# Performance work log

Measured on AMD Instinct MI355X. Metric: run time of the kernel, lower is better.

## Reference

```python
import jax, jax.numpy as jnp
import numpy as np
import math

N_LEVELS = 16
F = 2
LOG2_T = 19
T = 1 << LOG2_T  # 524288 hashmap rows
BASE, FINEST = 16, 512
# b computed in float32 like torch.exp((log(512)-log(16))/15)
B_GROWTH = float(np.exp((np.log(np.float32(FINEST)) - np.log(np.float32(BASE))) / np.float32(N_LEVELS - 1)))
RES = [math.floor(BASE * B_GROWTH ** i) for i in range(N_LEVELS)]
SIZES = [(r + 1) ** 3 if r ** 3 < T else T for r in RES]
OFFS = np.concatenate([[0], np.cumsum(SIZES)]).tolist()
TOTAL_ROWS = OFFS[-1]  # 5269629
# corner order (i,j,k) for i,j,k in {0,1}, i outermost -> matches torch grid_offset
CORNER_OFF = np.array([[i, j, k] for i in (0, 1) for j in (0, 1) for k in (0, 1)], dtype=np.int32)
PRIMES = np.array([1, 2654435761, 805459861], dtype=np.uint32)
N_POINTS = 1048576


def setup_inputs() -> dict:
    key = jax.random.key(0)
    k1, k2 = jax.random.split(key)
    x = jax.random.uniform(k1, (N_POINTS, 3), dtype=jnp.float32, minval=-1.0, maxval=1.0)
    # nn.init.uniform_(-1e-4, 1e-4) on every level's embedding table
    tables = jax.random.uniform(k2, (TOTAL_ROWS, F), dtype=jnp.float32, minval=-1e-4, maxval=1e-4)
    return {"x": x, "tables": tables}


def _level_embed(x, table, res):
    # x: (B,3) in [-1,1]; table: (rows,F); res: python int (static)
    xc = jnp.clip(x, -1.0, 1.0)
    grid = jnp.float32(2.0 / res)  # (box_max-box_min)/resolution
    bl = jnp.floor((xc + 1.0) / grid).astype(jnp.int32)  # (B,3) bottom-left voxel
    vmin = bl.astype(x.dtype) * grid - 1.0               # voxel_min_vertex
    # original uses unclamped x for interpolation weights
    w = (x - vmin) / grid                                # (B,3)
    corners = bl[:, None, :] + jnp.asarray(CORNER_OFF)   # (B,8,3)
    if res ** 3 < T:
        # one-to-one hash: i*res^2 + j*res + k
        idx = corners[..., 0] * (res * res) + corners[..., 1] * res + corners[..., 2]
    else:
        # spatial hash with uint32 wraparound multiplication (matches torch int32 wrap)
        c = corners.astype(jnp.uint32)
        h = (c[..., 0] * PRIMES[0]) ^ (c[..., 1] * PRIMES[1]) ^ (c[..., 2] * PRIMES[2])
        idx = (h & jnp.uint32(T - 1)).astype(jnp.int32)
    e = table[idx]  # (B,8,F) gather
    wx, wy, wz = w[:, 0:1], w[:, 1:2], w[:, 2:3]
    c00 = e[:, 0] * (1 - wx) + e[:, 4] * wx
    c01 = e[:, 1] * (1 - wx) + e[:, 5] * wx
    c10 = e[:, 2] * (1 - wx) + e[:, 6] * wx
    c11 = e[:, 3] * (1 - wx) + e[:, 7] * wx
    c0 = c00 * (1 - wy) + c10 * wy
    c1 = c01 * (1 - wy) + c11 * wy
    return c0 * (1 - wz) + c1 * wz  # (B,F)


def reference(x, tables):
    outs = []
    for i in range(N_LEVELS):
        tab = jax.lax.slice_in_dim(tables, OFFS[i], OFFS[i + 1], axis=0)
        outs.append(_level_embed(x, tab, RES[i]))
    return jnp.concatenate(outs, axis=-1)  # (B, n_levels*F) = (B,32)
```

## Files before the change

### kernel.cpp

```cpp
#include <hip/hip_runtime.h>

#define NLVL 16
#define T_MASK ((1u << 19) - 1)
#define NBIN 32768

typedef float v2f __attribute__((ext_vector_type(2)));
typedef float v4f __attribute__((ext_vector_type(4)));

__constant__ int c_res[NLVL] = {16, 20, 25, 32, 40, 50, 64, 80,
                                101, 128, 161, 203, 256, 322, 406, 512};
__constant__ int c_off[NLVL] = {0, 4913, 14174, 31750, 67687, 136608, 269259, 543884,
                                1075325, 1599613, 2123901, 2648189, 3172477, 3696765, 4221053, 4745341};
__constant__ float c_grid[NLVL] = {
    (float)(2.0 / 16.0),  (float)(2.0 / 20.0),  (float)(2.0 / 25.0),  (float)(2.0 / 32.0),
    (float)(2.0 / 40.0),  (float)(2.0 / 50.0),  (float)(2.0 / 64.0),  (float)(2.0 / 80.0),
    (float)(2.0 / 101.0), (float)(2.0 / 128.0), (float)(2.0 / 161.0), (float)(2.0 / 203.0),
    (float)(2.0 / 256.0), (float)(2.0 / 322.0), (float)(2.0 / 406.0), (float)(2.0 / 512.0)};

constexpr int kRes[8] = {16, 20, 25, 32, 40, 50, 64, 80};
constexpr int kOff[8] = {0, 4913, 14174, 31750, 67687, 136608, 269259, 543884};
constexpr float kGrid[8] = {
    (float)(2.0 / 16.0), (float)(2.0 / 20.0), (float)(2.0 / 25.0), (float)(2.0 / 32.0),
    (float)(2.0 / 40.0), (float)(2.0 / 50.0), (float)(2.0 / 64.0), (float)(2.0 / 80.0)};

__device__ __forceinline__ void dim_setup(float xv, float grid, int& b, float& w) {
    float xc = fminf(fmaxf(xv, -1.0f), 1.0f);
    float fb = floorf((xc + 1.0f) / grid);
    b = (int)fb;
    float vmin = fb * grid - 1.0f;
    w = (xv - vmin) / grid;
}

__device__ __forceinline__ unsigned part1by2(unsigned v) {
    v &= 0x3ff;
    v = (v | (v << 16)) & 0x030000FFu;
    v = (v | (v << 8))  & 0x0300F00Fu;
    v = (v | (v << 4))  & 0x030C30C3u;
    v = (v | (v << 2))  & 0x09249249u;
    return v;
}

__device__ __forceinline__ unsigned bin3(float a, float b, float c) {
    int ba = (int)floorf((a + 1.0f) * 16.0f); ba = ba < 0 ? 0 : (ba > 31 ? 31 : ba);
    int bb = (int)floorf((b + 1.0f) * 16.0f); bb = bb < 0 ? 0 : (bb > 31 ? 31 : bb);
    int bc = (int)floorf((c + 1.0f) * 16.0f); bc = bc < 0 ? 0 : (bc > 31 ? 31 : bc);
    return part1by2((unsigned)ba) | (part1by2((unsigned)bb) << 1) | (part1by2((unsigned)bc) << 2);
}

__global__ __launch_bounds__(256) void hist_kernel(const float* __restrict__ x,
                                                   unsigned* __restrict__ hist, int n) {
    int p = (int)blockIdx.x * 256 + (int)threadIdx.x;
    if (p >= n) return;
    float a = x[3 * p], b = x[3 * p + 1], c = x[3 * p + 2];
    atomicAdd(&hist[bin3(a, b, c)], 1u);
}

__global__ __launch_bounds__(1024) void scan_kernel(const unsigned* __restrict__ hist,
                                                    unsigned* __restrict__ base) {
    __shared__ unsigned part[1024];
    const int t = (int)threadIdx.x;
    unsigned s = 0;
#pragma unroll
    for (int i = 0; i < NBIN / 1024; ++i) s += hist[t * (NBIN / 1024) + i];
    part[t] = s;
    __syncthreads();
    for (int off = 1; off < 1024; off <<= 1) {
        unsigned v = (t >= off) ? part[t - off] : 0u;
        __syncthreads();
        part[t] += v;
        __syncthreads();
    }
    unsigned run = part[t] - s;
    for (int i = 0; i < NBIN / 1024; ++i) {
        unsigned h = hist[t * (NBIN / 1024) + i];
        base[t * (NBIN / 1024) + i] = run;
        run += h;
    }
}

__global__ __launch_bounds__(256) void scatter_kernel(const float* __restrict__ x,
                                                      unsigned* __restrict__ base,
                                                      v4f* __restrict__ pts, int n) {
    int p = (int)blockIdx.x * 256 + (int)threadIdx.x;
    if (p >= n) return;
    float a = x[3 * p], b = x[3 * p + 1], c = x[3 * p + 2];
    unsigned slot = atomicAdd(&base[bin3(a, b, c)], 1u);
    v4f v; v.x = a; v.y = b; v.z = c; v.w = __int_as_float(p);
    pts[slot] = v;
}

__global__ __launch_bounds__(256) void gather_hash(const v4f* __restrict__ pts,
                                                   const float* __restrict__ tables,
                                                   v2f* __restrict__ ws2, int n) {
    const int level = (int)(blockIdx.x & 7) + 8;
    const int p = (int)(blockIdx.x >> 3) * 256 + (int)threadIdx.x;
    if (p >= n) return;

    const v4f pt = __builtin_nontemporal_load(&pts[p]);
    const float grid = c_grid[level];
    const v2f* __restrict__ tab = reinterpret_cast<const v2f*>(tables) + c_off[level];

    int bx, by, bz;
    float wx, wy, wz;
    dim_setup(pt.x, grid, bx, wx);
    dim_setup(pt.y, grid, by, wy);
    dim_setup(pt.z, grid, bz, wz);

    const unsigned hx0 = (unsigned)bx, hx1 = (unsigned)(bx + 1);
    const unsigned hy0 = (unsigned)by * 2654435761u;
    const unsigned hy1 = (unsigned)(by + 1) * 2654435761u;
    const unsigned hz0 = (unsigned)bz * 805459861u;
    const unsigned hz1 = (unsigned)(bz + 1) * 805459861u;
    v2f e0 = tab[(hx0 ^ hy0 ^ hz0) & T_MASK];
    v2f e1 = tab[(hx0 ^ hy0 ^ hz1) & T_MASK];
    v2f e2 = tab[(hx0 ^ hy1 ^ hz0) & T_MASK];
    v2f e3 = tab[(hx0 ^ hy1 ^ hz1) & T_MASK];
    v2f e4 = tab[(hx1 ^ hy0 ^ hz0) & T_MASK];
    v2f e5 = tab[(hx1 ^ hy0 ^ hz1) & T_MASK];
    v2f e6 = tab[(hx1 ^ hy1 ^ hz0) & T_MASK];
    v2f e7 = tab[(hx1 ^ hy1 ^ hz1) & T_MASK];

    const float ox = 1.0f - wx, oy = 1.0f - wy, oz = 1.0f - wz;
    v2f c00 = e0 * ox + e4 * wx;
    v2f c01 = e1 * ox + e5 * wx;
    v2f c10 = e2 * ox + e6 * wx;
    v2f c11 = e3 * ox + e7 * wx;
    v2f c0 = c00 * oy + c10 * wy;
    v2f c1 = c01 * oy + c11 * wy;
    v2f r = c0 * oz + c1 * wz;

    __builtin_nontemporal_store(r, &ws2[(size_t)(level - 8) * n + p]);
}

#define ROWSTRIDE 36
__global__ __launch_bounds__(256, 4) void dense_finish(const v4f* __restrict__ pts,
                                                       const float* __restrict__ tables,
                                                       const v2f* __restrict__ ws2,
                                                       float* __restrict__ out, int n) {
    __shared__ float lrow[256 * ROWSTRIDE];
    __shared__ int lorg[256];

    const int nb = (int)gridDim.x;
    const int bid = (int)blockIdx.x;
    const int q = nb >> 3, r = nb & 7;
    const int xcd = bid & 7, j = bid >> 3;
    const int nbid = (xcd < r) ? xcd * (q + 1) + j : r * (q + 1) + (xcd - r) * q + j;
    const int tid = (int)threadIdx.x;
    const int base_p = nbid * 256;
    const int p = base_p + tid;

    if (p < n) {
        v2f h[8];
#pragma unroll
        for (int l = 0; l < 8; ++l)
            h[l] = __builtin_nontemporal_load(&ws2[(size_t)l * n + p]);

        const v4f pt = __builtin_nontemporal_load(&pts[p]);
        lorg[tid] = __float_as_int(pt.w);

        v2f d[8];
#pragma unroll
        for (int l = 0; l < 8; ++l) {
            const int res = kRes[l];
            const float grid = kGrid[l];
            const v2f* __restrict__ tab = reinterpret_cast<const v2f*>(tables) + kOff[l];
            int bx, by, bz;
            float wx, wy, wz;
            dim_setup(pt.x, grid, bx, wx);
            dim_setup(pt.y, grid, by, wy);
            dim_setup(pt.z, grid, bz, wz);
            const int r2 = res * res;
            const int base = bx * r2 + by * res + bz;
            v2f e0 = tab[base];            v2f e1 = tab[base + 1];
            v2f e2 = tab[base + res];      v2f e3 = tab[base + res + 1];
            v2f e4 = tab[base + r2];       v2f e5 = tab[base + r2 + 1];
            v2f e6 = tab[base + r2 + res]; v2f e7 = tab[base + r2 + res + 1];
            const float ox = 1.0f - wx, oy = 1.0f - wy, oz = 1.0f - wz;
            v2f c00 = e0 * ox + e4 * wx;
            v2f c01 = e1 * ox + e5 * wx;
            v2f c10 = e2 * ox + e6 * wx;
            v2f c11 = e3 * ox + e7 * wx;
            v2f c0 = c00 * oy + c10 * wy;
            v2f c1 = c01 * oy + c11 * wy;
            d[l] = c0 * oz + c1 * wz;
        }

        float* myrow = &lrow[tid * ROWSTRIDE];
#pragma unroll
        for (int k = 0; k < 4; ++k) {
            v4f v; v.x = d[2 * k].x; v.y = d[2 * k].y; v.z = d[2 * k + 1].x; v.w = d[2 * k + 1].y;
            *reinterpret_cast<v4f*>(myrow + 4 * k) = v;
        }
#pragma unroll
        for (int k = 0; k < 4; ++k) {
            v4f v; v.x = h[2 * k].x; v.y = h[2 * k].y; v.z = h[2 * k + 1].x; v.w = h[2 * k + 1].y;
            *reinterpret_cast<v4f*>(myrow + 16 + 4 * k) = v;
        }
    }
    __syncthreads();

    const int c = tid & 7;
    const int r0 = tid >> 3;
#pragma unroll
    for (int s = 0; s < 8; ++s) {
        const int rr = s * 32 + r0;
        if (base_p + rr < n) {
            v4f v = *reinterpret_cast<const v4f*>(&lrow[rr * ROWSTRIDE + c * 4]);
            const int o = lorg[rr];
            *reinterpret_cast<v4f*>(out + (size_t)o * 32 + c * 4) = v;
        }
    }
}

__global__ __launch_bounds__(256) void hashgrid_direct(const float* __restrict__ x,
                                                       const float* __restrict__ tables,
                                                       float* __restrict__ out, int n_points) {
    const int t = (int)blockIdx.x * 256 + (int)threadIdx.x;
    const int p = t >> 4;
    if (p >= n_points) return;
    const int l = t & 15;
    const float xx = x[p * 3 + 0], xy = x[p * 3 + 1], xz = x[p * 3 + 2];
    const int res = c_res[l];
    const float grid = c_grid[l];
    const v2f* __restrict__ tab = reinterpret_cast<const v2f*>(tables) + c_off[l];
    int bx, by, bz; float wx, wy, wz;
    dim_setup(xx, grid, bx, wx);
    dim_setup(xy, grid, by, wy);
    dim_setup(xz, grid, bz, wz);
    v2f e0, e1, e2, e3, e4, e5, e6, e7;
    if (l < 8) {
        const int r2 = res * res;
        const int base = bx * r2 + by * res + bz;
        e0 = tab[base];            e1 = tab[base + 1];
        e2 = tab[base + res];      e3 = tab[base + res + 1];
        e4 = tab[base + r2];       e5 = tab[base + r2 + 1];
        e6 = tab[base + r2 + res]; e7 = tab[base + r2 + res + 1];
    } else {
        const unsigned hx0 = (unsigned)bx, hx1 = (unsigned)(bx + 1);
        const unsigned hy0 = (unsigned)by * 2654435761u, hy1 = (unsigned)(by + 1) * 2654435761u;
        const unsigned hz0 = (unsigned)bz * 805459861u,  hz1 = (unsigned)(bz + 1) * 805459861u;
        e0 = tab[(hx0 ^ hy0 ^ hz0) & T_MASK]; e1 = tab[(hx0 ^ hy0 ^ hz1) & T_MASK];
        e2 = tab[(hx0 ^ hy1 ^ hz0) & T_MASK]; e3 = tab[(hx0 ^ hy1 ^ hz1) & T_MASK];
        e4 = tab[(hx1 ^ hy0 ^ hz0) & T_MASK]; e5 = tab[(hx1 ^ hy0 ^ hz1) & T_MASK];
        e6 = tab[(hx1 ^ hy1 ^ hz0) & T_MASK]; e7 = tab[(hx1 ^ hy1 ^ hz1) & T_MASK];
    }
    const float ox = 1.0f - wx, oy = 1.0f - wy, oz = 1.0f - wz;
    v2f c00 = e0 * ox + e4 * wx, c01 = e1 * ox + e5 * wx;
    v2f c10 = e2 * ox + e6 * wx, c11 = e3 * ox + e7 * wx;
    v2f c0 = c00 * oy + c10 * wy, c1 = c01 * oy + c11 * wy;
    v2f r = c0 * oz + c1 * wz;
    reinterpret_cast<v2f*>(out)[(size_t)p * NLVL + l] = r;
}

extern "C" void kernel_launch(void* const* d_in, const int* in_sizes, int n_in,
                              void* d_out, int out_size, void* d_ws, size_t ws_size,
                              hipStream_t stream) {
    const float* x = (const float*)d_in[0];
    const float* tables = (const float*)d_in[1];
    float* out = (float*)d_out;
    const int n = in_sizes[0] / 3;

    const size_t need = 262144 + (size_t)n * 16 + (size_t)n * 64;
    if (ws_size < need) {
        const int blocks = (n * NLVL + 255) / 256;
        hipLaunchKernelGGL(hashgrid_direct, dim3(blocks), dim3(256), 0, stream, x, tables, out, n);
        return;
    }

    char* w = (char*)d_ws;
    unsigned* hist = (unsigned*)w;
    unsigned* base = (unsigned*)(w + 131072);
    v4f* pts = (v4f*)(w + 262144);
    v2f* ws2 = (v2f*)(w + 262144 + (size_t)n * 16);

    const int pb = (n + 255) / 256;

    hipMemsetAsync(hist, 0, NBIN * sizeof(unsigned), stream);
    hipLaunchKernelGGL(hist_kernel, dim3(pb), dim3(256), 0, stream, x, hist, n);
    hipLaunchKernelGGL(scan_kernel, dim3(1), dim3(1024), 0, stream, hist, base);
    hipLaunchKernelGGL(scatter_kernel, dim3(pb), dim3(256), 0, stream, x, base, pts, n);

    hipLaunchKernelGGL(gather_hash, dim3(pb * 8), dim3(256), 0, stream, pts, tables, ws2, n);
    hipLaunchKernelGGL(dense_finish, dim3(pb), dim3(256), 0, stream, pts, tables, ws2, out, n);
}
```

Measured before the change: 430.4 us.

## Fuse histogram into hash gather on unsorted points and split output stores

The hashed-level gather now reads points in their original order, staging x through shared memory, and also does the binning histogram, so the separate hist kernel goes away. The hashed-level results are then written straight to their own output rows by a coalesced hash_store kernel, and dense_store only scatters the 16 dense-level columns through the sort permutation. The scan is rewritten with shared-memory per-thread serial sums. The trade-off is that hash gathers lose the spatial locality that sorting gave, and writing each output row in two half-row passes may cost write efficiency.

New measurement: 461.7 us. 7.3% more time.

```diff
diff --git a/kernel.cpp b/kernel.cpp
--- a/kernel.cpp
+++ b/kernel.cpp
@@ -47,64 +47,40 @@
     return part1by2((unsigned)ba) | (part1by2((unsigned)bb) << 1) | (part1by2((unsigned)bc) << 2);
 }
 
-__global__ __launch_bounds__(256) void hist_kernel(const float* __restrict__ x,
-                                                   unsigned* __restrict__ hist, int n) {
-    int p = (int)blockIdx.x * 256 + (int)threadIdx.x;
+__global__ __launch_bounds__(256) void gather_hash_u(const float* __restrict__ x,
+                                                     const float* __restrict__ tables,
+                                                     v2f* __restrict__ ws2,
+                                                     unsigned* __restrict__ hist, int n) {
+    __shared__ float sx[768];
+    const int level = (int)(blockIdx.x & 7) + 8;
+    const int chunk = (int)(blockIdx.x >> 3);
+    const int p0 = chunk * 256;
+    const int tid = (int)threadIdx.x;
+
+    for (int i = tid; i < 768; i += 256) {
+        int gi = p0 * 3 + i;
+        sx[i] = (gi < n * 3) ? x[gi] : 0.0f;
+    }
+    __syncthreads();
+
+    const int p = p0 + tid;
     if (p >= n) return;
-    float a = x[3 * p], b = x[3 * p + 1], c = x[3 * p + 2];
-    atomicAdd(&hist[bin3(a, b, c)], 1u);
-}
-
-__global__ __launch_bounds__(1024) void scan_kernel(const unsigned* __restrict__ hist,
-                                                    unsigned* __restrict__ base) {
-    __shared__ unsigned part[1024];
-    const int t = (int)threadIdx.x;
-    unsigned s = 0;
-#pragma unroll
-    for (int i = 0; i < NBIN / 1024; ++i) s += hist[t * (NBIN / 1024) + i];
-    part[t] = s;
-    __syncthreads();
-    for (int off = 1; off < 1024; off <<= 1) {
-        unsigned v = (t >= off) ? part[t - off] : 0u;
-        __syncthreads();
-        part[t] += v;
-        __syncthreads();
-    }
-    unsigned run = part[t] - s;
-    for (int i = 0; i < NBIN / 1024; ++i) {
-        unsigned h = hist[t * (NBIN / 1024) + i];
-        base[t * (NBIN / 1024) + i] = run;
-        run += h;
-    }
-}
-
-__global__ __launch_bounds__(256) void scatter_kernel(const float* __restrict__ x,
-                                                      unsigned* __restrict__ base,
-                                                      v4f* __restrict__ pts, int n) {
-    int p = (int)blockIdx.x * 256 + (int)threadIdx.x;
-    if (p >= n) return;
-    float a = x[3 * p], b = x[3 * p + 1], c = x[3 * p + 2];
-    unsigned slot = atomicAdd(&base[bin3(a, b, c)], 1u);
-    v4f v; v.x = a; v.y = b; v.z = c; v.w = __int_as_float(p);
-    pts[slot] = v;
-}
-
-__global__ __launch_bounds__(256) void gather_hash(const v4f* __restrict__ pts,
-                                                   const float* __restrict__ tables,
-                                                   v2f* __restrict__ ws2, int n) {
-    const int level = (int)(blockIdx.x & 7) + 8;
-    const int p = (int)(blockIdx.x >> 3) * 256 + (int)threadIdx.x;
-    if (p >= n) return;
-
-    const v4f pt = __builtin_nontemporal_load(&pts[p]);
+
+    const float xx = sx[tid * 3 + 0];
+    const float xy = sx[tid * 3 + 1];
+    const float xz = sx[tid * 3 + 2];
+
+    if ((int)(blockIdx.x & 7) == (chunk & 7))
+        atomicAdd(&hist[bin3(xx, xy, xz)], 1u);
+
     const float grid = c_grid[level];
     const v2f* __restrict__ tab = reinterpret_cast<const v2f*>(tables) + c_off[level];
 
     int bx, by, bz;
     float wx, wy, wz;
-    dim_setup(pt.x, grid, bx, wx);
-    dim_setup(pt.y, grid, by, wy);
-    dim_setup(pt.z, grid, bz, wz);
+    dim_setup(xx, grid, bx, wx);
+    dim_setup(xy, grid, by, wy);
+    dim_setup(xz, grid, bz, wz);
 
     const unsigned hx0 = (unsigned)bx, hx1 = (unsigned)(bx + 1);
     const unsigned hy0 = (unsigned)by * 2654435761u;
@@ -132,12 +108,62 @@
     __builtin_nontemporal_store(r, &ws2[(size_t)(level - 8) * n + p]);
 }
 
-#define ROWSTRIDE 36
-__global__ __launch_bounds__(256, 4) void dense_finish(const v4f* __restrict__ pts,
-                                                       const float* __restrict__ tables,
-                                                       const v2f* __restrict__ ws2,
-                                                       float* __restrict__ out, int n) {
-    __shared__ float lrow[256 * ROWSTRIDE];
+__global__ __launch_bounds__(1024) void scan_kernel(const unsigned* __restrict__ hist,
+                                                    unsigned* __restrict__ base) {
+    __shared__ unsigned lh[NBIN + NBIN / 32];
+    __shared__ unsigned part[1024];
+    __shared__ unsigned cbase[1024];
+    const int t = (int)threadIdx.x;
+
+#pragma unroll
+    for (int i = 0; i < NBIN / 1024; ++i) {
+        int g = i * 1024 + t;
+        lh[g + (g >> 5)] = hist[g];
+    }
+    __syncthreads();
+
+    unsigned run = 0;
+#pragma unroll
+    for (int i = 0; i < 32; ++i) {
+        unsigned v = lh[t * 33 + i];
+        lh[t * 33 + i] = run;
+        run += v;
+    }
+    part[t] = run;
+    __syncthreads();
+
+    for (int off = 1; off < 1024; off <<= 1) {
+        unsigned v = (t >= off) ? part[t - off] : 0u;
+        __syncthreads();
+        part[t] += v;
+        __syncthreads();
+    }
+    cbase[t] = part[t] - run;
+    __syncthreads();
+
+#pragma unroll
+    for (int i = 0; i < NBIN / 1024; ++i) {
+        int g = i * 1024 + t;
+        base[g] = lh[g + (g >> 5)] + cbase[g >> 5];
+    }
+}
+
+__global__ __launch_bounds__(256) void scatter_kernel(const float* __restrict__ x,
+                                                      unsigned* __restrict__ base,
+                                                      v4f* __restrict__ pts, int n) {
+    int p = (int)blockIdx.x * 256 + (int)threadIdx.x;
+    if (p >= n) return;
+    float a = x[3 * p], b = x[3 * p + 1], c = x[3 * p + 2];
+    unsigned slot = atomicAdd(&base[bin3(a, b, c)], 1u);
+    v4f v; v.x = a; v.y = b; v.z = c; v.w = __int_as_float(p);
+    pts[slot] = v;
+}
+
+#define RS2 20
+__global__ __launch_bounds__(256, 4) void dense_store(const v4f* __restrict__ pts,
+                                                      const float* __restrict__ tables,
+                                                      float* __restrict__ out, int n) {
+    __shared__ float lrow[256 * RS2];
     __shared__ int lorg[256];
 
     const int nb = (int)gridDim.x;
@@ -150,11 +176,6 @@
     const int p = base_p + tid;
 
     if (p < n) {
-        v2f h[8];
-#pragma unroll
-        for (int l = 0; l < 8; ++l)
-            h[l] = __builtin_nontemporal_load(&ws2[(size_t)l * n + p]);
-
         const v4f pt = __builtin_nontemporal_load(&pts[p]);
         lorg[tid] = __float_as_int(pt.w);
 
@@ -185,29 +206,55 @@
             d[l] = c0 * oz + c1 * wz;
         }
 
-        float* myrow = &lrow[tid * ROWSTRIDE];
+        float* myrow = &lrow[tid * RS2];
 #pragma unroll
         for (int k = 0; k < 4; ++k) {
             v4f v; v.x = d[2 * k].x; v.y = d[2 * k].y; v.z = d[2 * k + 1].x; v.w = d[2 * k + 1].y;
             *reinterpret_cast<v4f*>(myrow + 4 * k) = v;
         }
-#pragma unroll
-        for (int k = 0; k < 4; ++k) {
-            v4f v; v.x = h[2 * k].x; v.y = h[2 * k].y; v.z = h[2 * k + 1].x; v.w = h[2 * k + 1].y;
-            *reinterpret_cast<v4f*>(myrow + 16 + 4 * k) = v;
-        }
-    }
-    __syncthreads();
-
-    const int c = tid & 7;
-    const int r0 = tid >> 3;
-#pragma unroll
-    for (int s = 0; s < 8; ++s) {
-        const int rr = s * 32 + r0;
+    }
+    __syncthreads();
+
+    const int c = tid & 3;
+    const int r0 = tid >> 2;
+#pragma unroll
+    for (int s = 0; s < 4; ++s) {
+        const int rr = s * 64 + r0;
         if (base_p + rr < n) {
-            v4f v = *reinterpret_cast<const v4f*>(&lrow[rr * ROWSTRIDE + c * 4]);
+            v4f v = *reinterpret_cast<const v4f*>(&lrow[rr * RS2 + c * 4]);
             const int o = lorg[rr];
             *reinterpret_cast<v4f*>(out + (size_t)o * 32 + c * 4) = v;
+        }
+    }
+}
+
+__global__ __launch_bounds__(256) void hash_store(const v2f* __restrict__ ws2,
+                                                  float* __restrict__ out, int n) {
+    __shared__ float lrow[256 * RS2];
+    const int p0 = (int)blockIdx.x * 256;
+    const int tid = (int)threadIdx.x;
+    const int p = p0 + tid;
+
+    if (p < n) {
+        float* myrow = &lrow[tid * RS2];
+#pragma unroll
+        for (int l = 0; l < 4; ++l) {
+            v2f a = __builtin_nontemporal_load(&ws2[(size_t)(2 * l) * n + p]);
+            v2f b = __builtin_nontemporal_load(&ws2[(size_t)(2 * l + 1) * n + p]);
+            v4f v; v.x = a.x; v.y = a.y; v.z = b.x; v.w = b.y;
+            *reinterpret_cast<v4f*>(myrow + 4 * l) = v;
+        }
+    }
+    __syncthreads();
+
+    const int c = tid & 3;
+    const int r0 = tid >> 2;
+#pragma unroll
+    for (int s = 0; s < 4; ++s) {
+        const int rr = s * 64 + r0;
+        if (p0 + rr < n) {
+            v4f v = *reinterpret_cast<const v4f*>(&lrow[rr * RS2 + c * 4]);
+            *reinterpret_cast<v4f*>(out + (size_t)(p0 + rr) * 32 + 16 + c * 4) = v;
         }
     }
 }
@@ -276,10 +323,9 @@
     const int pb = (n + 255) / 256;
 
     hipMemsetAsync(hist, 0, NBIN * sizeof(unsigned), stream);
-    hipLaunchKernelGGL(hist_kernel, dim3(pb), dim3(256), 0, stream, x, hist, n);
+    hipLaunchKernelGGL(gather_hash_u, dim3(pb * 8), dim3(256), 0, stream, x, tables, ws2, hist, n);
     hipLaunchKernelGGL(scan_kernel, dim3(1), dim3(1024), 0, stream, hist, base);
     hipLaunchKernelGGL(scatter_kernel, dim3(pb), dim3(256), 0, stream, x, base, pts, n);
-
-    hipLaunchKernelGGL(gather_hash, dim3(pb * 8), dim3(256), 0, stream, pts, tables, ws2, n);
-    hipLaunchKernelGGL(dense_finish, dim3(pb), dim3(256), 0, stream, pts, tables, ws2, out, n);
-}
+    hipLaunchKernelGGL(dense_store, dim3(pb), dim3(256), 0, stream, pts, tables, out, n);
+    hipLaunchKernelGGL(hash_store, dim3(pb), dim3(256), 0, stream, ws2, out, n);
+}
```

## Switch sorted points to SoA, stage x in LDS, and scan histogram in shared memory

Applied to the files above, without the earlier changes.

The sorted point buffer changes from an interleaved float4 array to separate x, y, z and original-index arrays, read by the gather and finish kernels. The histogram and scatter kernels now load the interleaved input into LDS with coalesced reads before binning. The single-block scan copies the histogram into padded shared memory so its serial per-thread pass avoids strided global reads. The SoA layout makes the scatter issue four scattered 4-byte stores per point instead of one 16-byte store, and the gather kernels issue three loads instead of one vector load.

After: 398.3 us. -7.5%, faster.

```diff
diff --git a/kernel.cpp b/kernel.cpp
--- a/kernel.cpp
+++ b/kernel.cpp
@@ -49,62 +49,98 @@
 
 __global__ __launch_bounds__(256) void hist_kernel(const float* __restrict__ x,
                                                    unsigned* __restrict__ hist, int n) {
-    int p = (int)blockIdx.x * 256 + (int)threadIdx.x;
+    __shared__ float lx[768];
+    const int p0 = (int)blockIdx.x * 256;
+    const int tid = (int)threadIdx.x;
+    for (int i = tid; i < 768; i += 256) {
+        int gi = p0 * 3 + i;
+        lx[i] = (gi < n * 3) ? x[gi] : 0.0f;
+    }
+    __syncthreads();
+    const int p = p0 + tid;
     if (p >= n) return;
-    float a = x[3 * p], b = x[3 * p + 1], c = x[3 * p + 2];
-    atomicAdd(&hist[bin3(a, b, c)], 1u);
+    atomicAdd(&hist[bin3(lx[3 * tid], lx[3 * tid + 1], lx[3 * tid + 2])], 1u);
 }
 
 __global__ __launch_bounds__(1024) void scan_kernel(const unsigned* __restrict__ hist,
                                                     unsigned* __restrict__ base) {
+    __shared__ unsigned lh[NBIN + NBIN / 32];
     __shared__ unsigned part[1024];
+    __shared__ unsigned cbase[1024];
     const int t = (int)threadIdx.x;
-    unsigned s = 0;
-#pragma unroll
-    for (int i = 0; i < NBIN / 1024; ++i) s += hist[t * (NBIN / 1024) + i];
-    part[t] = s;
-    __syncthreads();
+
+#pragma unroll
+    for (int i = 0; i < NBIN / 1024; ++i) {
+        int g = i * 1024 + t;
+        lh[g + (g >> 5)] = hist[g];
+    }
+    __syncthreads();
+
+    unsigned run = 0;
+#pragma unroll
+    for (int i = 0; i < 32; ++i) {
+        unsigned v = lh[t * 33 + i];
+        lh[t * 33 + i] = run;
+        run += v;
+    }
+    part[t] = run;
+    __syncthreads();
+
     for (int off = 1; off < 1024; off <<= 1) {
         unsigned v = (t >= off) ? part[t - off] : 0u;
         __syncthreads();
         part[t] += v;
         __syncthreads();
     }
-    unsigned run = part[t] - s;
+    cbase[t] = part[t] - run;
+    __syncthreads();
+
+#pragma unroll
     for (int i = 0; i < NBIN / 1024; ++i) {
-        unsigned h = hist[t * (NBIN / 1024) + i];
-        base[t * (NBIN / 1024) + i] = run;
-        run += h;
+        int g = i * 1024 + t;
+        base[g] = lh[g + (g >> 5)] + cbase[g >> 5];
     }
 }
 
 __global__ __launch_bounds__(256) void scatter_kernel(const float* __restrict__ x,
                                                       unsigned* __restrict__ base,
-                                                      v4f* __restrict__ pts, int n) {
-    int p = (int)blockIdx.x * 256 + (int)threadIdx.x;
+                                                      float* __restrict__ sx,
+                                                      float* __restrict__ sy,
+                                                      float* __restrict__ sz,
+                                                      int* __restrict__ org, int n) {
+    __shared__ float lx[768];
+    const int p0 = (int)blockIdx.x * 256;
+    const int tid = (int)threadIdx.x;
+    for (int i = tid; i < 768; i += 256) {
+        int gi = p0 * 3 + i;
+        lx[i] = (gi < n * 3) ? x[gi] : 0.0f;
+    }
+    __syncthreads();
+    const int p = p0 + tid;
     if (p >= n) return;
-    float a = x[3 * p], b = x[3 * p + 1], c = x[3 * p + 2];
+    float a = lx[3 * tid], b = lx[3 * tid + 1], c = lx[3 * tid + 2];
     unsigned slot = atomicAdd(&base[bin3(a, b, c)], 1u);
-    v4f v; v.x = a; v.y = b; v.z = c; v.w = __int_as_float(p);
-    pts[slot] = v;
-}
-
-__global__ __launch_bounds__(256) void gather_hash(const v4f* __restrict__ pts,
+    sx[slot] = a; sy[slot] = b; sz[slot] = c; org[slot] = p;
+}
+
+__global__ __launch_bounds__(256) void gather_hash(const float* __restrict__ sx,
+                                                   const float* __restrict__ sy,
+                                                   const float* __restrict__ sz,
                                                    const float* __restrict__ tables,
                                                    v2f* __restrict__ ws2, int n) {
     const int level = (int)(blockIdx.x & 7) + 8;
     const int p = (int)(blockIdx.x >> 3) * 256 + (int)threadIdx.x;
     if (p >= n) return;
 
-    const v4f pt = __builtin_nontemporal_load(&pts[p]);
+    const float xx = sx[p], xy = sy[p], xz = sz[p];
     const float grid = c_grid[level];
     const v2f* __restrict__ tab = reinterpret_cast<const v2f*>(tables) + c_off[level];
 
     int bx, by, bz;
     float wx, wy, wz;
-    dim_setup(pt.x, grid, bx, wx);
-    dim_setup(pt.y, grid, by, wy);
-    dim_setup(pt.z, grid, bz, wz);
+    dim_setup(xx, grid, bx, wx);
+    dim_setup(xy, grid, by, wy);
+    dim_setup(xz, grid, bz, wz);
 
     const unsigned hx0 = (unsigned)bx, hx1 = (unsigned)(bx + 1);
     const unsigned hy0 = (unsigned)by * 2654435761u;
@@ -133,7 +169,10 @@
 }
 
 #define ROWSTRIDE 36
-__global__ __launch_bounds__(256, 4) void dense_finish(const v4f* __restrict__ pts,
+__global__ __launch_bounds__(256, 4) void dense_finish(const float* __restrict__ sx,
+                                                       const float* __restrict__ sy,
+                                                       const float* __restrict__ sz,
+                                                       const int* __restrict__ org,
                                                        const float* __restrict__ tables,
                                                        const v2f* __restrict__ ws2,
                                                        float* __restrict__ out, int n) {
@@ -155,8 +194,10 @@
         for (int l = 0; l < 8; ++l)
             h[l] = __builtin_nontemporal_load(&ws2[(size_t)l * n + p]);
 
-        const v4f pt = __builtin_nontemporal_load(&pts[p]);
-        lorg[tid] = __float_as_int(pt.w);
+        const float xx = __builtin_nontemporal_load(&sx[p]);
+        const float xy = __builtin_nontemporal_load(&sy[p]);
+        const float xz = __builtin_nontemporal_load(&sz[p]);
+        lorg[tid] = __builtin_nontemporal_load(&org[p]);
 
         v2f d[8];
 #pragma unroll
@@ -166,9 +207,9 @@
             const v2f* __restrict__ tab = reinterpret_cast<const v2f*>(tables) + kOff[l];
             int bx, by, bz;
             float wx, wy, wz;
-            dim_setup(pt.x, grid, bx, wx);
-            dim_setup(pt.y, grid, by, wy);
-            dim_setup(pt.z, grid, bz, wz);
+            dim_setup(xx, grid, bx, wx);
+            dim_setup(xy, grid, by, wy);
+            dim_setup(xz, grid, bz, wz);
             const int r2 = res * res;
             const int base = bx * r2 + by * res + bz;
             v2f e0 = tab[base];            v2f e1 = tab[base + 1];
@@ -270,7 +311,10 @@
     char* w = (char*)d_ws;
     unsigned* hist = (unsigned*)w;
     unsigned* base = (unsigned*)(w + 131072);
-    v4f* pts = (v4f*)(w + 262144);
+    float* sx = (float*)(w + 262144);
+    float* sy = sx + n;
+    float* sz = sy + n;
+    int* org = (int*)(sz + n);
     v2f* ws2 = (v2f*)(w + 262144 + (size_t)n * 16);
 
     const int pb = (n + 255) / 256;
@@ -278,8 +322,7 @@
     hipMemsetAsync(hist, 0, NBIN * sizeof(unsigned), stream);
     hipLaunchKernelGGL(hist_kernel, dim3(pb), dim3(256), 0, stream, x, hist, n);
     hipLaunchKernelGGL(scan_kernel, dim3(1), dim3(1024), 0, stream, hist, base);
-    hipLaunchKernelGGL(scatter_kernel, dim3(pb), dim3(256), 0, stream, x, base, pts, n);
-
-    hipLaunchKernelGGL(gather_hash, dim3(pb * 8), dim3(256), 0, stream, pts, tables, ws2, n);
-    hipLaunchKernelGGL(dense_finish, dim3(pb), dim3(256), 0, stream, pts, tables, ws2, out, n);
-}
+    hipLaunchKernelGGL(scatter_kernel, dim3(pb), dim3(256), 0, stream, x, base, sx, sy, sz, org, n);
+    hipLaunchKernelGGL(gather_hash, dim3(pb * 8), dim3(256), 0, stream, sx, sy, sz, tables, ws2, n);
+    hipLaunchKernelGGL(dense_finish, dim3(pb), dim3(256), 0, stream, sx, sy, sz, org, tables, ws2, out, n);
+}
```
